# Optimization experiments

Measured on AMD Instinct MI355X. Metric: run time of the kernel, lower is better.

Reference implementation:

```python
import jax, jax.numpy as jnp
import numpy as np

NUM_NODES = 50000
NUM_EDGES = 800000
IN_CH = 64
HID = 64
SEQ = 8
K = 3
LAMBDA_MAX = 2.0  # PyG ChebConv default lambda_max for 'sym' normalization


def setup_inputs() -> dict:
    key = jax.random.key(0)
    ks = jax.random.split(key, 16)
    X = jax.random.normal(ks[0], (1, SEQ, NUM_NODES, IN_CH), dtype=jnp.float32)
    edge_index = jax.random.randint(ks[1], (2, NUM_EDGES), 0, NUM_NODES)
    edge_weight = jax.random.uniform(ks[2], (NUM_EDGES,), dtype=jnp.float32)

    def wb(i, cin):
        W = jax.random.normal(ks[3 + i], (K, cin, HID), dtype=jnp.float32) * 0.05
        b = jnp.zeros((HID,), dtype=jnp.float32)
        return W, b

    W_xz, b_xz = wb(0, IN_CH); W_hz, b_hz = wb(1, HID)
    W_xr, b_xr = wb(2, IN_CH); W_hr, b_hr = wb(3, HID)
    W_xh, b_xh = wb(4, IN_CH); W_hh, b_hh = wb(5, HID)
    return dict(X=X, edge_index=edge_index, edge_weight=edge_weight,
                W_xz=W_xz, b_xz=b_xz, W_hz=W_hz, b_hz=b_hz,
                W_xr=W_xr, b_xr=b_xr, W_hr=W_hr, b_hr=b_hr,
                W_xh=W_xh, b_xh=b_xh, W_hh=W_hh, b_hh=b_hh)


def _cheb_norm(edge_index, edge_weight, n):
    # Scaled Laplacian L_hat = (2/lambda_max) * (I - D^-1/2 A D^-1/2) - I
    row, col = edge_index[0], edge_index[1]
    w = jnp.where(row == col, 0.0, edge_weight)  # remove self loops (PyG does)
    deg = jax.ops.segment_sum(w, row, num_segments=n)
    dinv = jnp.where(deg > 0, jax.lax.rsqrt(jnp.where(deg > 0, deg, 1.0)), 0.0)
    wn = -(2.0 / LAMBDA_MAX) * w * dinv[row] * dinv[col]  # off-diagonal entries
    diag = 2.0 / LAMBDA_MAX - 1.0  # diagonal entry (0 for sym, lambda_max=2)
    return row, col, wn, diag


def _cheb_conv(x, W, b, row, col, wn, diag):
    # Chebyshev recurrence: T0 = x, T1 = L_hat x, T_k = 2 L_hat T_{k-1} - T_{k-2}
    n = x.shape[0]

    def prop(v):  # sparse L_hat @ v
        return jax.ops.segment_sum(wn[:, None] * v[col], row, num_segments=n) + diag * v

    out = x @ W[0]
    Tx_prev, Tx = x, prop(x)
    out = out + Tx @ W[1]
    for k in range(2, W.shape[0]):
        Tx_prev, Tx = Tx, 2.0 * prop(Tx) - Tx_prev
        out = out + Tx @ W[k]
    return out + b


def _gconv_gru(X, edge_index, edge_weight, params):
    B, L, N, C = X.shape
    row, col, wn, diag = _cheb_norm(edge_index, edge_weight, B * N)
    (W_xz, b_xz, W_hz, b_hz, W_xr, b_xr, W_hr, b_hr, W_xh, b_xh, W_hh, b_hh) = params
    hid = W_xz.shape[2]
    H0 = jnp.zeros((B * N, hid), dtype=X.dtype)

    def cc(v, W, b):
        return _cheb_conv(v, W, b, row, col, wn, diag)

    def step(H, Xt):  # Xt: [B, N, C] flattened per original reshape
        Xf = Xt.reshape(B * N, C)
        Z = jax.nn.sigmoid(cc(Xf, W_xz, b_xz) + cc(H, W_hz, b_hz))
        R = jax.nn.sigmoid(cc(Xf, W_xr, b_xr) + cc(H, W_hr, b_hr))
        Ht = jnp.tanh(cc(Xf, W_xh, b_xh) + cc(H * R, W_hh, b_hh))
        Hn = Z * H + (1.0 - Z) * Ht
        return Hn, Hn

    Hlast, states = jax.lax.scan(step, H0, jnp.moveaxis(X, 1, 0))
    States = jnp.moveaxis(states.reshape(L, B, N, hid), 0, 1)  # [B, L, N, hid]
    return States, Hlast.reshape(B, N, hid)


def reference(X, edge_index, edge_weight, W_xz, b_xz, W_hz, b_hz, W_xr, b_xr,
              W_hr, b_hr, W_xh, b_xh, W_hh, b_hh):
    params = (W_xz, b_xz, W_hz, b_hz, W_xr, b_xr, W_hr, b_hr, W_xh, b_xh, W_hh, b_hh)
    return _gconv_gru(X, edge_index, edge_weight, params)
```

## Files before the change

kernel.cpp:

```cpp
#include <hip/hip_runtime.h>
#include <cmath>

#define SEQLEN 8
#define CH 64

typedef unsigned short ushort_t;
typedef __attribute__((ext_vector_type(8))) short bf16x8;
typedef __attribute__((ext_vector_type(4))) float f32x4;

__device__ __forceinline__ ushort_t f2bf(float f) {
  union { float f; unsigned u; } v; v.f = f;
  unsigned r = v.u + 0x7fff + ((v.u >> 16) & 1);
  return (ushort_t)(r >> 16);
}
__device__ __forceinline__ float bf2f(ushort_t h) {
  union { unsigned u; float f; } v; v.u = ((unsigned)h) << 16;
  return v.f;
}

__global__ __launch_bounds__(256) void edge_hist_kernel(
    const int* __restrict__ ei, const float* __restrict__ ew,
    float* __restrict__ deg, int* __restrict__ cnt, int E) {
  int e = blockIdx.x * 256 + threadIdx.x;
  if (e >= E) return;
  int r = ei[e];
  int c = ei[E + e];
  float wv = (r == c) ? 0.f : ew[e];
  atomicAdd(deg + r, wv);
  atomicAdd(cnt + r, 1);
}

__global__ __launch_bounds__(256) void dinv_kernel(
    const float* __restrict__ deg, float* __restrict__ dinv, int n) {
  int i = blockIdx.x * 256 + threadIdx.x;
  if (i >= n) return;
  float d = deg[i];
  dinv[i] = (d > 0.f) ? (1.0f / sqrtf(d)) : 0.f;
}

__global__ __launch_bounds__(256) void scan_part_kernel(
    const int* __restrict__ cnt, int* __restrict__ bsum, int n) {
  int i = blockIdx.x * 256 + threadIdx.x;
  int v = (i < n) ? cnt[i] : 0;
#pragma unroll
  for (int o = 32; o; o >>= 1) v += __shfl_down(v, o, 64);
  __shared__ int red[4];
  if ((threadIdx.x & 63) == 0) red[threadIdx.x >> 6] = v;
  __syncthreads();
  if (threadIdx.x == 0) bsum[blockIdx.x] = red[0] + red[1] + red[2] + red[3];
}

__global__ __launch_bounds__(256) void scan_top_kernel(int* __restrict__ bsum, int nb) {
  int tid = threadIdx.x, lane = tid & 63, wid = tid >> 6;
  int v = (tid < nb) ? bsum[tid] : 0;
  int orig = v;
#pragma unroll
  for (int o = 1; o < 64; o <<= 1) { int t = __shfl_up(v, o, 64); if (lane >= o) v += t; }
  __shared__ int wsum[4];
  if (lane == 63) wsum[wid] = v;
  __syncthreads();
  int base = 0;
  for (int w = 0; w < wid; ++w) base += wsum[w];
  if (tid < nb) bsum[tid] = base + v - orig;
}

__global__ __launch_bounds__(256) void scan_fill_kernel(
    const int* __restrict__ cnt, const int* __restrict__ bsum,
    int* __restrict__ rowp, int* __restrict__ woff, int n, int total) {
  int i = blockIdx.x * 256 + threadIdx.x;
  int tid = threadIdx.x, lane = tid & 63, wid = tid >> 6;
  int v = (i < n) ? cnt[i] : 0;
  int orig = v;
#pragma unroll
  for (int o = 1; o < 64; o <<= 1) { int t = __shfl_up(v, o, 64); if (lane >= o) v += t; }
  __shared__ int wsum[4];
  if (lane == 63) wsum[wid] = v;
  __syncthreads();
  int base = bsum[blockIdx.x];
  for (int w = 0; w < wid; ++w) base += wsum[w];
  if (i < n) { int ex = base + v - orig; rowp[i] = ex; woff[i] = ex; }
  if (blockIdx.x == 0 && tid == 0) rowp[n] = total;
}

__global__ __launch_bounds__(256) void scatter_kernel(
    const int* __restrict__ ei, const float* __restrict__ ew,
    const float* __restrict__ dinv, int* __restrict__ woff,
    int* __restrict__ ccol, float* __restrict__ cwn, int E) {
  int e = blockIdx.x * 256 + threadIdx.x;
  if (e >= E) return;
  int r = ei[e];
  int c = ei[E + e];
  float wv = (r == c) ? 0.f : ew[e];
  float wn = -wv * dinv[r] * dinv[c];
  int pos = atomicAdd(woff + r, 1);
  ccol[pos] = c;
  cwn[pos] = wn;
}

__global__ __launch_bounds__(256) void cvt_bt_kernel(
    const float* __restrict__ X, ushort_t* __restrict__ Xt,
    long long NF, long long total4) {
  long long i = (long long)blockIdx.x * 256 + threadIdx.x;
  if (i >= total4) return;
  long long e4 = i * 4;
  int node = (int)(e4 >> 9);
  int rem = (int)(e4 & 511);
  int slab = rem >> 6;
  int cb = rem & 63;
  const float* src = X + (size_t)slab * NF + (size_t)node * CH + cb;
  float4 v = *(const float4*)src;
  ushort4 o;
  o.x = f2bf(v.x); o.y = f2bf(v.y); o.z = f2bf(v.z); o.w = f2bf(v.w);
  *(ushort4*)(Xt + e4) = o;
}

__global__ __launch_bounds__(256) void cvt_wt_kernel(
    const float* __restrict__ W, ushort_t* __restrict__ Wt) {
  int i = blockIdx.x * 256 + threadIdx.x;
  if (i >= 3 * 4096) return;
  int kk = i >> 12, rem = i & 4095, c = rem >> 6, k = rem & 63;
  Wt[i] = f2bf(W[(kk << 12) + (k << 6) + c]);
}

__global__ __launch_bounds__(256) void spmv_kernel(
    const int* __restrict__ rowp, const int* __restrict__ ccol,
    const float* __restrict__ cwn, const float* __restrict__ v,
    const float* __restrict__ u, float* __restrict__ y,
    float alpha, float beta, int n, long long slab_stride) {
  int r = blockIdx.x * 4 + (threadIdx.x >> 6);
  if (r >= n) return;
  long long so = (long long)blockIdx.y * slab_stride;
  const float* __restrict__ vs = v + so;
  const float* __restrict__ us = u + so;
  float* __restrict__ ys = y + so;
  int lane = threadIdx.x & 63;
  int s = __builtin_amdgcn_readfirstlane(rowp[r]);
  int e = __builtin_amdgcn_readfirstlane(rowp[r + 1]);
  float a0 = 0.f, a1 = 0.f, a2 = 0.f, a3 = 0.f;
  int i = s;
  for (; i + 4 <= e; i += 4) {
    int c0 = ccol[i], c1 = ccol[i + 1], c2 = ccol[i + 2], c3 = ccol[i + 3];
    float w0 = cwn[i], w1 = cwn[i + 1], w2 = cwn[i + 2], w3 = cwn[i + 3];
    float x0 = vs[(size_t)c0 * CH + lane];
    float x1 = vs[(size_t)c1 * CH + lane];
    float x2 = vs[(size_t)c2 * CH + lane];
    float x3 = vs[(size_t)c3 * CH + lane];
    a0 = fmaf(w0, x0, a0); a1 = fmaf(w1, x1, a1);
    a2 = fmaf(w2, x2, a2); a3 = fmaf(w3, x3, a3);
  }
  for (; i < e; ++i) a0 = fmaf(cwn[i], vs[(size_t)ccol[i] * CH + lane], a0);
  float res = alpha * ((a0 + a1) + (a2 + a3));
  if (beta != 0.f) res += beta * us[(size_t)r * CH + lane];
  ys[(size_t)r * CH + lane] = res;
}

__global__ __launch_bounds__(256) void spmv_bt_kernel(
    const int* __restrict__ rowp, const int* __restrict__ ccol,
    const float* __restrict__ cwn, const ushort_t* __restrict__ v,
    const float* __restrict__ u, ushort_t* __restrict__ yt,
    float alpha, float beta, int n, long long NF) {
  int r = blockIdx.x * 4 + (threadIdx.x >> 6);
  if (r >= n) return;
  int lane = threadIdx.x & 63;
  int s = __builtin_amdgcn_readfirstlane(rowp[r]);
  int e = __builtin_amdgcn_readfirstlane(rowp[r + 1]);
  float acc[8];
#pragma unroll
  for (int k = 0; k < 8; ++k) acc[k] = 0.f;
  const ushort_t* __restrict__ vl = v + (size_t)lane * 8;
  for (int i = s; i < e; i += 16) {
    int idxl = i + (lane & 15);
    int last = e - 1;
    if (idxl > last) idxl = last;
    int cL = ccol[idxl];
    float wL = cwn[idxl];
    int jv = e - i;
#pragma unroll
    for (int j = 0; j < 16; ++j) {
      int cj = __builtin_amdgcn_readlane(cL, j);
      int wb = __builtin_amdgcn_readlane(__float_as_int(wL), j);
      float wj = (j < jv) ? __int_as_float(wb) : 0.f;
      union { float4 f4; ushort_t us[8]; } tt;
      tt.f4 = *(const float4*)(vl + (size_t)cj * (SEQLEN * CH));
#pragma unroll
      for (int k = 0; k < 8; ++k)
        acc[k] = fmaf(wj, bf2f(tt.us[k]), acc[k]);
    }
  }
  float res[8];
#pragma unroll
  for (int k = 0; k < 8; ++k) res[k] = alpha * acc[k];
  if (beta != 0.f) {
    const float* up = u + (size_t)(lane >> 3) * NF + (size_t)r * CH + (size_t)(lane & 7) * 8;
    float4 ua = *(const float4*)up;
    float4 ub = *(const float4*)(up + 4);
    res[0] += beta * ua.x; res[1] += beta * ua.y; res[2] += beta * ua.z; res[3] += beta * ua.w;
    res[4] += beta * ub.x; res[5] += beta * ub.y; res[6] += beta * ub.z; res[7] += beta * ub.w;
  }
  union { float4 f4; ushort_t us[8]; } o;
#pragma unroll
  for (int k = 0; k < 8; ++k) o.us[k] = f2bf(res[k]);
  *(float4*)(yt + (size_t)r * (SEQLEN * CH) + (size_t)lane * 8) = o.f4;
}

__global__ __launch_bounds__(256) void spmv_bfx_kernel(
    const int* __restrict__ rowp, const int* __restrict__ ccol,
    const float* __restrict__ cwn, const ushort_t* __restrict__ v,
    const float* __restrict__ u, float* __restrict__ y, ushort_t* __restrict__ yb,
    float alpha, float beta, int n) {
  int r = blockIdx.x * 4 + (threadIdx.x >> 6);
  if (r >= n) return;
  int lane = threadIdx.x & 63;
  int s = __builtin_amdgcn_readfirstlane(rowp[r]);
  int e = __builtin_amdgcn_readfirstlane(rowp[r + 1]);
  float a0 = 0.f, a1 = 0.f, a2 = 0.f, a3 = 0.f;
  for (int i = s; i < e; i += 16) {
    int idxl = i + (lane & 15);
    int last = e - 1;
    if (idxl > last) idxl = last;
    int cL = ccol[idxl];
    float wL = cwn[idxl];
    int jv = e - i;
#pragma unroll
    for (int j = 0; j < 16; ++j) {
      int cj = __builtin_amdgcn_readlane(cL, j);
      int wb = __builtin_amdgcn_readlane(__float_as_int(wL), j);
      float wj = (j < jv) ? __int_as_float(wb) : 0.f;
      float xv = bf2f(v[(size_t)cj * CH + lane]);
      if ((j & 3) == 0) a0 = fmaf(wj, xv, a0);
      else if ((j & 3) == 1) a1 = fmaf(wj, xv, a1);
      else if ((j & 3) == 2) a2 = fmaf(wj, xv, a2);
      else a3 = fmaf(wj, xv, a3);
    }
  }
  float res = alpha * ((a0 + a1) + (a2 + a3));
  if (beta != 0.f) res += beta * u[(size_t)r * CH + lane];
  size_t oi = (size_t)r * CH + lane;
  if (y) y[oi] = res;
  if (yb) yb[oi] = f2bf(res);
}

__device__ __forceinline__ float sigf(float x) { return 1.f / (1.f + expf(-x)); }

struct FGM {
  const ushort_t* AB[3];
  const ushort_t* WB[3];
  const float* Bv[3];
  const float* P[2];
  const float* Hb;
  const float* Zb;
  float* O[3];
  ushort_t* OB0;
  int n;
  long long abstride;
};

template <int MODE, int G>
__global__ __launch_bounds__(256) void gemm_mfma_kernel(FGM p) {
  const int tid = threadIdx.x;
  const int wave = tid >> 6, lane = tid & 63;
  const int lr = lane & 15, kg = lane >> 4;
  const int wrow = blockIdx.x * 128 + wave * 32;
  f32x4 acc[G][2][4];
#pragma unroll
  for (int g = 0; g < G; ++g)
#pragma unroll
    for (int m = 0; m < 2; ++m)
#pragma unroll
      for (int ct = 0; ct < 4; ++ct) acc[g][m][ct] = (f32x4)0.f;

#pragma unroll
  for (int kk = 0; kk < 3; ++kk) {
    const ushort_t* __restrict__ Ab = p.AB[kk];
    bf16x8 a[2][2];
#pragma unroll
    for (int m = 0; m < 2; ++m) {
      int nn = wrow + m * 16 + lr;
      if (nn >= p.n) nn = p.n - 1;
      const ushort_t* ap = Ab + (size_t)nn * p.abstride + kg * 8;
      a[m][0] = *(const bf16x8*)(ap);
      a[m][1] = *(const bf16x8*)(ap + 32);
    }
#pragma unroll
    for (int g = 0; g < G; ++g) {
      const ushort_t* __restrict__ Wg = p.WB[g] + kk * 4096 + lr * 64 + kg * 8;
#pragma unroll
      for (int ct = 0; ct < 4; ++ct) {
        bf16x8 b0 = *(const bf16x8*)(Wg + ct * 1024);
        bf16x8 b1 = *(const bf16x8*)(Wg + ct * 1024 + 32);
        acc[g][0][ct] = __builtin_amdgcn_mfma_f32_16x16x32_bf16(a[0][0], b0, acc[g][0][ct], 0, 0, 0);
        acc[g][0][ct] = __builtin_amdgcn_mfma_f32_16x16x32_bf16(a[0][1], b1, acc[g][0][ct], 0, 0, 0);
        acc[g][1][ct] = __builtin_amdgcn_mfma_f32_16x16x32_bf16(a[1][0], b0, acc[g][1][ct], 0, 0, 0);
        acc[g][1][ct] = __builtin_amdgcn_mfma_f32_16x16x32_bf16(a[1][1], b1, acc[g][1][ct], 0, 0, 0);
      }
    }
  }

  if (MODE == 0) {
#pragma unroll
    for (int g = 0; g < G; ++g) {
#pragma unroll
      for (int ct = 0; ct < 4; ++ct) {
        int col = ct * 16 + lr;
        float bv = p.Bv[g][col];
#pragma unroll
        for (int m = 0; m < 2; ++m) {
#pragma unroll
          for (int i = 0; i < 4; ++i) {
            int row = wrow + m * 16 + kg * 4 + i;
            if (row < p.n) p.O[g][(size_t)row * CH + col] = acc[g][m][ct][i] + bv;
          }
        }
      }
    }
  } else if (MODE == 1) {
#pragma unroll
    for (int ct = 0; ct < 4; ++ct) {
      int col = ct * 16 + lr;
      float bz = p.Bv[0][col];
      float br = p.Bv[1][col];
#pragma unroll
      for (int m = 0; m < 2; ++m) {
#pragma unroll
        for (int i = 0; i < 4; ++i) {
          int row = wrow + m * 16 + kg * 4 + i;
          if (row < p.n) {
            size_t idx = (size_t)row * CH + col;
            float z = sigf(p.P[0][idx] + bz + acc[0][m][ct][i]);
            float gg = p.Hb[idx] * sigf(p.P[1][idx] + br + acc[1][m][ct][i]);
            p.O[0][idx] = z;
            p.O[1][idx] = gg;
            if (p.OB0) p.OB0[idx] = f2bf(gg);
          }
        }
      }
    }
  } else {
#pragma unroll
    for (int ct = 0; ct < 4; ++ct) {
      int col = ct * 16 + lr;
      float bh = p.Bv[0][col];
#pragma unroll
      for (int m = 0; m < 2; ++m) {
#pragma unroll
        for (int i = 0; i < 4; ++i) {
          int row = wrow + m * 16 + kg * 4 + i;
          if (row < p.n) {
            size_t idx = (size_t)row * CH + col;
            float tv = tanhf(p.P[0][idx] + bh + acc[0][m][ct][i]);
            float z4 = p.Zb[idx];
            float o = z4 * p.Hb[idx] + (1.f - z4) * tv;
            p.O[0][idx] = o;
            if (p.OB0) p.OB0[idx] = f2bf(o);
          }
        }
      }
    }
  }
}

struct FG {
  const float* A[3];
  const float* W[3];
  const float* Bv[3];
  const float* P[3];
  const float* Hb;
  const float* Zb;
  float* O[3];
  int n;
};

__device__ __forceinline__ void fma_tile(float (&acc)[4][4], const float* At,
                                         const float* Wt, int r0, int c0) {
#pragma unroll 4
  for (int k = 0; k < 64; ++k) {
    float4 a = *(const float4*)(At + k * 68 + r0);
    float4 w = *(const float4*)(Wt + k * 64 + c0);
    float av[4] = { a.x, a.y, a.z, a.w };
    float wv[4] = { w.x, w.y, w.z, w.w };
#pragma unroll
    for (int i = 0; i < 4; ++i)
#pragma unroll
      for (int j = 0; j < 4; ++j)
        acc[i][j] = fmaf(av[i], wv[j], acc[i][j]);
  }
}

template <int MODE, int G>
__global__ __launch_bounds__(256) void gemmf_kernel(FG p) {
  __shared__ float At[64 * 68];
  __shared__ float Wt[64 * 64];
  const int tid = threadIdx.x;
  const int n0 = blockIdx.x * 64;
  const int r0 = (tid >> 4) << 2;
  const int c0 = (tid & 15) << 2;
  float acc[G][4][4];
#pragma unroll
  for (int g = 0; g < G; ++g)
#pragma unroll
    for (int i = 0; i < 4; ++i)
#pragma unroll
      for (int j = 0; j < 4; ++j) acc[g][i][j] = 0.f;

  for (int kk = 0; kk < 3; ++kk) {
    const float* __restrict__ A = p.A[kk];
    __syncthreads();
#pragma unroll
    for (int j = 0; j < 4; ++j) {
      int flat = tid + 256 * j;
      int r = flat >> 4;
      int k4 = (flat & 15) << 2;
      int nn = n0 + r;
      float4 av = (nn < p.n) ? *(const float4*)(A + (size_t)nn * CH + k4)
                             : make_float4(0.f, 0.f, 0.f, 0.f);
      At[(k4 + 0) * 68 + r] = av.x;
      At[(k4 + 1) * 68 + r] = av.y;
      At[(k4 + 2) * 68 + r] = av.z;
      At[(k4 + 3) * 68 + r] = av.w;
    }
#pragma unroll
    for (int g = 0; g < G; ++g) {
      if (g > 0) __syncthreads();
      const float* __restrict__ Wk = p.W[g] + kk * 4096;
#pragma unroll
      for (int j = 0; j < 4; ++j) {
        int flat = tid + 256 * j;
        *(float4*)(Wt + flat * 4) = *(const float4*)(Wk + flat * 4);
      }
      __syncthreads();
      fma_tile(acc[g], At, Wt, r0, c0);
    }
  }

  if (MODE == 0) {
#pragma unroll
    for (int g = 0; g < G; ++g) {
      float4 bv = *(const float4*)(p.Bv[g] + c0);
#pragma unroll
      for (int i = 0; i < 4; ++i) {
        int nn = n0 + r0 + i;
        if (nn < p.n) {
          float4 o;
          o.x = acc[g][i][0] + bv.x;
          o.y = acc[g][i][1] + bv.y;
          o.z = acc[g][i][2] + bv.z;
          o.w = acc[g][i][3] + bv.w;
          *(float4*)(p.O[g] + (size_t)nn * CH + c0) = o;
        }
      }
    }
  } else if (MODE == 1) {
    float4 bz = *(const float4*)(p.Bv[0] + c0);
    float4 br = *(const float4*)(p.Bv[1] + c0);
#pragma unroll
    for (int i = 0; i < 4; ++i) {
      int nn = n0 + r0 + i;
      if (nn < p.n) {
        size_t idx = (size_t)nn * CH + c0;
        float4 pz = *(const float4*)(p.P[0] + idx);
        float4 pr = *(const float4*)(p.P[1] + idx);
        float4 h4 = *(const float4*)(p.Hb + idx);
        float4 z, gg;
        z.x = sigf(pz.x + bz.x + acc[0][i][0]);
        z.y = sigf(pz.y + bz.y + acc[0][i][1]);
        z.z = sigf(pz.z + bz.z + acc[0][i][2]);
        z.w = sigf(pz.w + bz.w + acc[0][i][3]);
        gg.x = h4.x * sigf(pr.x + br.x + acc[1][i][0]);
        gg.y = h4.y * sigf(pr.y + br.y + acc[1][i][1]);
        gg.z = h4.z * sigf(pr.z + br.z + acc[1][i][2]);
        gg.w = h4.w * sigf(pr.w + br.w + acc[1][i][3]);
        *(float4*)(p.O[0] + idx) = z;
        *(float4*)(p.O[1] + idx) = gg;
      }
    }
  } else {
    float4 bh = *(const float4*)(p.Bv[0] + c0);
#pragma unroll
    for (int i = 0; i < 4; ++i) {
      int nn = n0 + r0 + i;
      if (nn < p.n) {
        size_t idx = (size_t)nn * CH + c0;
        float4 ph = *(const float4*)(p.P[0] + idx);
        float4 z4 = *(const float4*)(p.Zb + idx);
        float4 h4 = *(const float4*)(p.Hb + idx);
        float4 o;
        float t0 = tanhf(ph.x + bh.x + acc[0][i][0]);
        float t1 = tanhf(ph.y + bh.y + acc[0][i][1]);
        float t2 = tanhf(ph.z + bh.z + acc[0][i][2]);
        float t3 = tanhf(ph.w + bh.w + acc[0][i][3]);
        o.x = z4.x * h4.x + (1.f - z4.x) * t0;
        o.y = z4.y * h4.y + (1.f - z4.y) * t1;
        o.z = z4.z * h4.z + (1.f - z4.z) * t2;
        o.w = z4.w * h4.w + (1.f - z4.w) * t3;
        *(float4*)(p.O[0] + idx) = o;
      }
    }
  }
}

__global__ __launch_bounds__(256) void t0_kernel(
    const float4* __restrict__ xzp, const float4* __restrict__ xhp,
    const float* __restrict__ b_hz, const float* __restrict__ b_hh,
    float4* __restrict__ out0, ushort_t* __restrict__ out0b, int n4) {
  int i = blockIdx.x * 256 + threadIdx.x;
  if (i >= n4) return;
  int cb = (i << 2) & 63;
  float4 bz = *(const float4*)(b_hz + cb);
  float4 bh = *(const float4*)(b_hh + cb);
  float4 z4 = xzp[i], h4 = xhp[i];
  float4 o;
  o.x = (1.f - sigf(z4.x + bz.x)) * tanhf(h4.x + bh.x);
  o.y = (1.f - sigf(z4.y + bz.y)) * tanhf(h4.y + bh.y);
  o.z = (1.f - sigf(z4.z + bz.z)) * tanhf(h4.z + bh.z);
  o.w = (1.f - sigf(z4.w + bz.w)) * tanhf(h4.w + bh.w);
  out0[i] = o;
  if (out0b) {
    ushort4 ob;
    ob.x = f2bf(o.x); ob.y = f2bf(o.y); ob.z = f2bf(o.z); ob.w = f2bf(o.w);
    *(ushort4*)(out0b + (size_t)i * 4) = ob;
  }
}

extern "C" void kernel_launch(void* const* d_in, const int* in_sizes, int n_in,
                              void* d_out, int out_size, void* d_ws, size_t ws_size,
                              hipStream_t stream) {
  const float* X    = (const float*)d_in[0];
  const int*   ei   = (const int*)d_in[1];
  const float* ewt  = (const float*)d_in[2];
  const float* W_xz = (const float*)d_in[3];  const float* b_xz = (const float*)d_in[4];
  const float* W_hz = (const float*)d_in[5];  const float* b_hz = (const float*)d_in[6];
  const float* W_xr = (const float*)d_in[7];  const float* b_xr = (const float*)d_in[8];
  const float* W_hr = (const float*)d_in[9];  const float* b_hr = (const float*)d_in[10];
  const float* W_xh = (const float*)d_in[11]; const float* b_xh = (const float*)d_in[12];
  const float* W_hh = (const float*)d_in[13]; const float* b_hh = (const float*)d_in[14];

  const int N = in_sizes[0] / (SEQLEN * CH);
  const int E = in_sizes[1] / 2;
  const size_t NF = (size_t)N * CH;
  float* out = (float*)d_out;

  char* base = (char*)d_ws;
  size_t off = 0;
  auto take = [&](size_t bytes) -> void* {
    off = (off + 255) & ~(size_t)255;
    void* p = base + off;
    off += bytes;
    return p;
  };
  float* deg   = (float*)take((size_t)N * 4);
  float* dinv  = (float*)take((size_t)N * 4);
  int*   cnt   = (int*)take((size_t)N * 4);
  int*   rowp  = (int*)take((size_t)(N + 1) * 4);
  int*   woff  = (int*)take((size_t)(N + 1) * 4);
  int*   bsum  = (int*)take(1024 * 4);
  int*   ccol  = (int*)take((size_t)E * 4);
  float* cwn   = (float*)take((size_t)E * 4);
  float* t1    = (float*)take(NF * 4);
  float* t2    = (float*)take(NF * 4);
  float* xz    = (float*)take(NF * 4);
  float* xr    = (float*)take(NF * 4);
  float* xh    = (float*)take(NF * 4);
  float* Gb    = (float*)take(NF * 4);
  ushort_t* Xb   = (ushort_t*)take(NF * 2 * SEQLEN);
  ushort_t* t1xb = (ushort_t*)take(NF * 2 * SEQLEN);
  ushort_t* t2xb = (ushort_t*)take(NF * 2 * SEQLEN);
  ushort_t* Hbb  = (ushort_t*)take(NF * 2);
  ushort_t* Gbb  = (ushort_t*)take(NF * 2);
  ushort_t* t1b  = (ushort_t*)take(NF * 2);
  ushort_t* t2b  = (ushort_t*)take(NF * 2);
  ushort_t* Wxzb = (ushort_t*)take(3 * 4096 * 2);
  ushort_t* Wxrb = (ushort_t*)take(3 * 4096 * 2);
  ushort_t* Wxhb = (ushort_t*)take(3 * 4096 * 2);
  ushort_t* Whzb = (ushort_t*)take(3 * 4096 * 2);
  ushort_t* Whrb = (ushort_t*)take(3 * 4096 * 2);
  ushort_t* Whhb = (ushort_t*)take(3 * 4096 * 2);
  size_t off_bf = off;
  (void)n_in; (void)out_size;
  const bool useBF = (off_bf <= ws_size);

  hipMemsetAsync(deg, 0, (size_t)N * 4, stream);
  hipMemsetAsync(cnt, 0, (size_t)N * 4, stream);

  const int ebl = (E + 255) / 256;
  const int nbl = (N + 255) / 256;
  edge_hist_kernel<<<ebl, 256, 0, stream>>>(ei, ewt, deg, cnt, E);
  dinv_kernel<<<nbl, 256, 0, stream>>>(deg, dinv, N);
  scan_part_kernel<<<nbl, 256, 0, stream>>>(cnt, bsum, N);
  scan_top_kernel<<<1, 256, 0, stream>>>(bsum, nbl);
  scan_fill_kernel<<<nbl, 256, 0, stream>>>(cnt, bsum, rowp, woff, N, E);
  scatter_kernel<<<ebl, 256, 0, stream>>>(ei, ewt, dinv, woff, ccol, cwn, E);

  const int nq = (N + 3) / 4;
  const int g3x = (N + 63) / 64;
  const int gmx = (N + 127) / 128;
  const int n4 = (int)(NF / 4);
  const int ewbl = (n4 + 255) / 256;

  if (useBF) {
    cvt_wt_kernel<<<48, 256, 0, stream>>>(W_xz, Wxzb);
    cvt_wt_kernel<<<48, 256, 0, stream>>>(W_xr, Wxrb);
    cvt_wt_kernel<<<48, 256, 0, stream>>>(W_xh, Wxhb);
    cvt_wt_kernel<<<48, 256, 0, stream>>>(W_hz, Whzb);
    cvt_wt_kernel<<<48, 256, 0, stream>>>(W_hr, Whrb);
    cvt_wt_kernel<<<48, 256, 0, stream>>>(W_hh, Whhb);

    long long xn4 = (long long)(NF * SEQLEN / 4);
    cvt_bt_kernel<<<(int)((xn4 + 255) / 256), 256, 0, stream>>>(X, Xb, (long long)NF, xn4);
    spmv_bt_kernel<<<dim3(nq, 1), 256, 0, stream>>>(
        rowp, ccol, cwn, Xb, nullptr, t1xb, 1.f, 0.f, N, (long long)NF);
    spmv_bt_kernel<<<dim3(nq, 1), 256, 0, stream>>>(
        rowp, ccol, cwn, t1xb, X, t2xb, 2.f, -1.f, N, (long long)NF);

    for (int t = 0; t < SEQLEN; ++t) {
      float* outt = out + (size_t)t * NF;

      FGM px = {};
      px.AB[0] = Xb + (size_t)t * CH;
      px.AB[1] = t1xb + (size_t)t * CH;
      px.AB[2] = t2xb + (size_t)t * CH;
      px.WB[0] = Wxzb; px.WB[1] = Wxrb; px.WB[2] = Wxhb;
      px.Bv[0] = b_xz; px.Bv[1] = b_xr; px.Bv[2] = b_xh;
      px.O[0] = xz; px.O[1] = xr; px.O[2] = xh;
      px.n = N; px.abstride = SEQLEN * CH;
      gemm_mfma_kernel<0, 3><<<dim3(gmx, 1, 1), 256, 0, stream>>>(px);

      if (t == 0) {
        t0_kernel<<<ewbl, 256, 0, stream>>>((const float4*)xz, (const float4*)xh,
                                            b_hz, b_hh, (float4*)outt, Hbb, n4);
        continue;
      }
      const float* H = out + (size_t)(t - 1) * NF;

      spmv_bfx_kernel<<<dim3(nq, 1), 256, 0, stream>>>(rowp, ccol, cwn, Hbb, H, t1, t1b, 1.f, 0.f, N);
      spmv_bfx_kernel<<<dim3(nq, 1), 256, 0, stream>>>(rowp, ccol, cwn, t1b, H, t2, t2b, 2.f, -1.f, N);
      FGM ph = {};
      ph.AB[0] = Hbb; ph.AB[1] = t1b; ph.AB[2] = t2b;
      ph.WB[0] = Whzb; ph.WB[1] = Whrb;
      ph.Bv[0] = b_hz; ph.Bv[1] = b_hr;
      ph.P[0] = xz; ph.P[1] = xr;
      ph.Hb = H;
      ph.O[0] = xz;
      ph.O[1] = Gb;
      ph.OB0 = Gbb;
      ph.n = N; ph.abstride = CH;
      gemm_mfma_kernel<1, 2><<<dim3(gmx, 1, 1), 256, 0, stream>>>(ph);

      spmv_bfx_kernel<<<dim3(nq, 1), 256, 0, stream>>>(rowp, ccol, cwn, Gbb, Gb, t1, t1b, 1.f, 0.f, N);
      spmv_bfx_kernel<<<dim3(nq, 1), 256, 0, stream>>>(rowp, ccol, cwn, t1b, Gb, t2, t2b, 2.f, -1.f, N);
      FGM pg = {};
      pg.AB[0] = Gbb; pg.AB[1] = t1b; pg.AB[2] = t2b;
      pg.WB[0] = Whhb;
      pg.Bv[0] = b_hh;
      pg.P[0] = xh;
      pg.Zb = xz;
      pg.Hb = H;
      pg.O[0] = outt;
      pg.OB0 = (t < SEQLEN - 1) ? Hbb : nullptr;
      pg.n = N; pg.abstride = CH;
      gemm_mfma_kernel<2, 1><<<dim3(gmx, 1, 1), 256, 0, stream>>>(pg);
    }
  } else {
    for (int t = 0; t < SEQLEN; ++t) {
      const float* Xt = X + (size_t)t * NF;
      float* outt = out + (size_t)t * NF;

      spmv_kernel<<<dim3(nq, 1), 256, 0, stream>>>(rowp, ccol, cwn, Xt, Xt, t1, 1.f, 0.f, N, 0);
      spmv_kernel<<<dim3(nq, 1), 256, 0, stream>>>(rowp, ccol, cwn, t1, Xt, t2, 2.f, -1.f, N, 0);
      FG px = {};
      px.A[0] = Xt; px.A[1] = t1; px.A[2] = t2;
      px.W[0] = W_xz; px.W[1] = W_xr; px.W[2] = W_xh;
      px.Bv[0] = b_xz; px.Bv[1] = b_xr; px.Bv[2] = b_xh;
      px.O[0] = xz; px.O[1] = xr; px.O[2] = xh;
      px.n = N;
      gemmf_kernel<0, 3><<<dim3(g3x, 1, 1), 256, 0, stream>>>(px);

      if (t == 0) {
        t0_kernel<<<ewbl, 256, 0, stream>>>((const float4*)xz, (const float4*)xh,
                                            b_hz, b_hh, (float4*)outt, nullptr, n4);
        continue;
      }
      const float* H = out + (size_t)(t - 1) * NF;

      spmv_kernel<<<dim3(nq, 1), 256, 0, stream>>>(rowp, ccol, cwn, H, H, t1, 1.f, 0.f, N, 0);
      spmv_kernel<<<dim3(nq, 1), 256, 0, stream>>>(rowp, ccol, cwn, t1, H, t2, 2.f, -1.f, N, 0);
      FG ph = {};
      ph.A[0] = H; ph.A[1] = t1; ph.A[2] = t2;
      ph.W[0] = W_hz; ph.W[1] = W_hr;
      ph.Bv[0] = b_hz; ph.Bv[1] = b_hr;
      ph.P[0] = xz; ph.P[1] = xr;
      ph.Hb = H;
      ph.O[0] = xz;
      ph.O[1] = Gb;
      ph.n = N;
      gemmf_kernel<1, 2><<<dim3(g3x, 1, 1), 256, 0, stream>>>(ph);

      spmv_kernel<<<dim3(nq, 1), 256, 0, stream>>>(rowp, ccol, cwn, Gb, Gb, t1, 1.f, 0.f, N, 0);
      spmv_kernel<<<dim3(nq, 1), 256, 0, stream>>>(rowp, ccol, cwn, t1, Gb, t2, 2.f, -1.f, N, 0);
      FG pg = {};
      pg.A[0] = Gb; pg.A[1] = t1; pg.A[2] = t2;
      pg.W[0] = W_hh;
      pg.Bv[0] = b_hh;
      pg.P[0] = xh;
      pg.Zb = xz;
      pg.Hb = H;
      pg.O[0] = outt;
      pg.n = N;
      gemmf_kernel<2, 1><<<dim3(g3x, 1, 1), 256, 0, stream>>>(pg);
    }
  }

  hipMemcpyAsync(out + (size_t)SEQLEN * NF, out + (size_t)(SEQLEN - 1) * NF,
                 NF * 4, hipMemcpyDeviceToDevice, stream);
}
```

Baseline: 2.071 ms.

## Fuse input-side Chebyshev GEMMs into the hidden-state gate GEMM kernels

Removes the separate per-step input GEMM that wrote xz/xr/xh to fp32 buffers. The X-side Chebyshev products are now accumulated directly in the same MFMA accumulators as the H-side products inside the gate kernels, and t=0 gets its own fused kernel that replaces t0_kernel. The SpMV calls also stop writing the unused fp32 t1/t2 outputs. This trades extra X-operand loads and MFMAs in each gate kernel for fewer launches and less fp32 intermediate traffic.

```diff
diff --git a/kernel.cpp b/kernel.cpp
--- a/kernel.cpp
+++ b/kernel.cpp
@@ -242,21 +242,24 @@
 
 __device__ __forceinline__ float sigf(float x) { return 1.f / (1.f + expf(-x)); }
 
-struct FGM {
-  const ushort_t* AB[3];
-  const ushort_t* WB[3];
-  const float* Bv[3];
-  const float* P[2];
+struct FGF {
+  const ushort_t* ABx[3];
+  const ushort_t* ABh[3];
+  const ushort_t* WX[2];
+  const ushort_t* WH[2];
+  const float* BX[2];
+  const float* BH[2];
   const float* Hb;
   const float* Zb;
-  float* O[3];
-  ushort_t* OB0;
+  float* O0;
+  float* O1;
+  ushort_t* OB;
   int n;
-  long long abstride;
 };
 
-template <int MODE, int G>
-__global__ __launch_bounds__(256) void gemm_mfma_kernel(FGM p) {
+template <int MODE>
+__global__ __launch_bounds__(256) void gemm_fused_kernel(FGF p) {
+  constexpr int G = (MODE == 2) ? 1 : 2;
   const int tid = threadIdx.x;
   const int wave = tid >> 6, lane = tid & 63;
   const int lr = lane & 15, kg = lane >> 4;
@@ -269,21 +272,19 @@
 #pragma unroll
       for (int ct = 0; ct < 4; ++ct) acc[g][m][ct] = (f32x4)0.f;
 
+  int nn0 = wrow + lr;       if (nn0 >= p.n) nn0 = p.n - 1;
+  int nn1 = wrow + 16 + lr;  if (nn1 >= p.n) nn1 = p.n - 1;
+
 #pragma unroll
   for (int kk = 0; kk < 3; ++kk) {
-    const ushort_t* __restrict__ Ab = p.AB[kk];
     bf16x8 a[2][2];
-#pragma unroll
-    for (int m = 0; m < 2; ++m) {
-      int nn = wrow + m * 16 + lr;
-      if (nn >= p.n) nn = p.n - 1;
-      const ushort_t* ap = Ab + (size_t)nn * p.abstride + kg * 8;
-      a[m][0] = *(const bf16x8*)(ap);
-      a[m][1] = *(const bf16x8*)(ap + 32);
-    }
+    const ushort_t* a0p = p.ABx[kk] + (size_t)nn0 * (SEQLEN * CH) + kg * 8;
+    const ushort_t* a1p = p.ABx[kk] + (size_t)nn1 * (SEQLEN * CH) + kg * 8;
+    a[0][0] = *(const bf16x8*)(a0p); a[0][1] = *(const bf16x8*)(a0p + 32);
+    a[1][0] = *(const bf16x8*)(a1p); a[1][1] = *(const bf16x8*)(a1p + 32);
 #pragma unroll
     for (int g = 0; g < G; ++g) {
-      const ushort_t* __restrict__ Wg = p.WB[g] + kk * 4096 + lr * 64 + kg * 8;
+      const ushort_t* __restrict__ Wg = p.WX[g] + kk * 4096 + lr * 64 + kg * 8;
 #pragma unroll
       for (int ct = 0; ct < 4; ++ct) {
         bf16x8 b0 = *(const bf16x8*)(Wg + ct * 1024);
@@ -296,65 +297,81 @@
     }
   }
 
-  if (MODE == 0) {
-#pragma unroll
-    for (int g = 0; g < G; ++g) {
-#pragma unroll
-      for (int ct = 0; ct < 4; ++ct) {
-        int col = ct * 16 + lr;
-        float bv = p.Bv[g][col];
-#pragma unroll
-        for (int m = 0; m < 2; ++m) {
-#pragma unroll
-          for (int i = 0; i < 4; ++i) {
-            int row = wrow + m * 16 + kg * 4 + i;
-            if (row < p.n) p.O[g][(size_t)row * CH + col] = acc[g][m][ct][i] + bv;
-          }
+  if (MODE != 0) {
+#pragma unroll
+    for (int kk = 0; kk < 3; ++kk) {
+      bf16x8 a[2][2];
+      const ushort_t* a0p = p.ABh[kk] + (size_t)nn0 * CH + kg * 8;
+      const ushort_t* a1p = p.ABh[kk] + (size_t)nn1 * CH + kg * 8;
+      a[0][0] = *(const bf16x8*)(a0p); a[0][1] = *(const bf16x8*)(a0p + 32);
+      a[1][0] = *(const bf16x8*)(a1p); a[1][1] = *(const bf16x8*)(a1p + 32);
+#pragma unroll
+      for (int g = 0; g < G; ++g) {
+        const ushort_t* __restrict__ Wg = p.WH[g] + kk * 4096 + lr * 64 + kg * 8;
+#pragma unroll
+        for (int ct = 0; ct < 4; ++ct) {
+          bf16x8 b0 = *(const bf16x8*)(Wg + ct * 1024);
+          bf16x8 b1 = *(const bf16x8*)(Wg + ct * 1024 + 32);
+          acc[g][0][ct] = __builtin_amdgcn_mfma_f32_16x16x32_bf16(a[0][0], b0, acc[g][0][ct], 0, 0, 0);
+          acc[g][0][ct] = __builtin_amdgcn_mfma_f32_16x16x32_bf16(a[0][1], b1, acc[g][0][ct], 0, 0, 0);
+          acc[g][1][ct] = __builtin_amdgcn_mfma_f32_16x16x32_bf16(a[1][0], b0, acc[g][1][ct], 0, 0, 0);
+          acc[g][1][ct] = __builtin_amdgcn_mfma_f32_16x16x32_bf16(a[1][1], b1, acc[g][1][ct], 0, 0, 0);
         }
       }
     }
-  } else if (MODE == 1) {
-#pragma unroll
-    for (int ct = 0; ct < 4; ++ct) {
-      int col = ct * 16 + lr;
-      float bz = p.Bv[0][col];
-      float br = p.Bv[1][col];
-#pragma unroll
-      for (int m = 0; m < 2; ++m) {
+  }
+
+#pragma unroll
+  for (int ct = 0; ct < 4; ++ct) {
+    int col = ct * 16 + lr;
+    if (MODE == 0) {
+      float bz = p.BX[0][col] + p.BH[0][col];
+      float bh = p.BX[1][col] + p.BH[1][col];
+#pragma unroll
+      for (int m = 0; m < 2; ++m)
 #pragma unroll
         for (int i = 0; i < 4; ++i) {
           int row = wrow + m * 16 + kg * 4 + i;
           if (row < p.n) {
             size_t idx = (size_t)row * CH + col;
-            float z = sigf(p.P[0][idx] + bz + acc[0][m][ct][i]);
-            float gg = p.Hb[idx] * sigf(p.P[1][idx] + br + acc[1][m][ct][i]);
-            p.O[0][idx] = z;
-            p.O[1][idx] = gg;
-            if (p.OB0) p.OB0[idx] = f2bf(gg);
+            float o = (1.f - sigf(acc[0][m][ct][i] + bz)) * tanhf(acc[1][m][ct][i] + bh);
+            p.O0[idx] = o;
+            p.OB[idx] = f2bf(o);
           }
         }
-      }
-    }
-  } else {
-#pragma unroll
-    for (int ct = 0; ct < 4; ++ct) {
-      int col = ct * 16 + lr;
-      float bh = p.Bv[0][col];
-#pragma unroll
-      for (int m = 0; m < 2; ++m) {
+    } else if (MODE == 1) {
+      float bz = p.BX[0][col] + p.BH[0][col];
+      float br = p.BX[1][col] + p.BH[1][col];
+#pragma unroll
+      for (int m = 0; m < 2; ++m)
 #pragma unroll
         for (int i = 0; i < 4; ++i) {
           int row = wrow + m * 16 + kg * 4 + i;
           if (row < p.n) {
             size_t idx = (size_t)row * CH + col;
-            float tv = tanhf(p.P[0][idx] + bh + acc[0][m][ct][i]);
-            float z4 = p.Zb[idx];
-            float o = z4 * p.Hb[idx] + (1.f - z4) * tv;
-            p.O[0][idx] = o;
-            if (p.OB0) p.OB0[idx] = f2bf(o);
+            float z = sigf(acc[0][m][ct][i] + bz);
+            float gg = p.Hb[idx] * sigf(acc[1][m][ct][i] + br);
+            p.O0[idx] = z;
+            p.O1[idx] = gg;
+            p.OB[idx] = f2bf(gg);
           }
         }
-      }
+    } else {
+      float bh = p.BX[0][col] + p.BH[0][col];
+#pragma unroll
+      for (int m = 0; m < 2; ++m)
+#pragma unroll
+        for (int i = 0; i < 4; ++i) {
+          int row = wrow + m * 16 + kg * 4 + i;
+          if (row < p.n) {
+            size_t idx = (size_t)row * CH + col;
+            float tv = tanhf(acc[0][m][ct][i] + bh);
+            float z = p.Zb[idx];
+            float o = z * p.Hb[idx] + (1.f - z) * tv;
+            p.O0[idx] = o;
+            if (p.OB) p.OB[idx] = f2bf(o);
+          }
+        }
     }
   }
 }
@@ -613,51 +630,56 @@
 
     for (int t = 0; t < SEQLEN; ++t) {
       float* outt = out + (size_t)t * NF;
-
-      FGM px = {};
-      px.AB[0] = Xb + (size_t)t * CH;
-      px.AB[1] = t1xb + (size_t)t * CH;
-      px.AB[2] = t2xb + (size_t)t * CH;
-      px.WB[0] = Wxzb; px.WB[1] = Wxrb; px.WB[2] = Wxhb;
-      px.Bv[0] = b_xz; px.Bv[1] = b_xr; px.Bv[2] = b_xh;
-      px.O[0] = xz; px.O[1] = xr; px.O[2] = xh;
-      px.n = N; px.abstride = SEQLEN * CH;
-      gemm_mfma_kernel<0, 3><<<dim3(gmx, 1, 1), 256, 0, stream>>>(px);
+      const ushort_t* Xs0 = Xb + (size_t)t * CH;
+      const ushort_t* Xs1 = t1xb + (size_t)t * CH;
+      const ushort_t* Xs2 = t2xb + (size_t)t * CH;
 
       if (t == 0) {
-        t0_kernel<<<ewbl, 256, 0, stream>>>((const float4*)xz, (const float4*)xh,
-                                            b_hz, b_hh, (float4*)outt, Hbb, n4);
+        FGF p0 = {};
+        p0.ABx[0] = Xs0; p0.ABx[1] = Xs1; p0.ABx[2] = Xs2;
+        p0.WX[0] = Wxzb; p0.WX[1] = Wxhb;
+        p0.BX[0] = b_xz; p0.BX[1] = b_xh;
+        p0.BH[0] = b_hz; p0.BH[1] = b_hh;
+        p0.O0 = outt; p0.OB = Hbb;
+        p0.n = N;
+        gemm_fused_kernel<0><<<dim3(gmx, 1, 1), 256, 0, stream>>>(p0);
         continue;
       }
       const float* H = out + (size_t)(t - 1) * NF;
 
-      spmv_bfx_kernel<<<dim3(nq, 1), 256, 0, stream>>>(rowp, ccol, cwn, Hbb, H, t1, t1b, 1.f, 0.f, N);
-      spmv_bfx_kernel<<<dim3(nq, 1), 256, 0, stream>>>(rowp, ccol, cwn, t1b, H, t2, t2b, 2.f, -1.f, N);
-      FGM ph = {};
-      ph.AB[0] = Hbb; ph.AB[1] = t1b; ph.AB[2] = t2b;
-      ph.WB[0] = Whzb; ph.WB[1] = Whrb;
-      ph.Bv[0] = b_hz; ph.Bv[1] = b_hr;
-      ph.P[0] = xz; ph.P[1] = xr;
-      ph.Hb = H;
-      ph.O[0] = xz;
-      ph.O[1] = Gb;
-      ph.OB0 = Gbb;
-      ph.n = N; ph.abstride = CH;
-      gemm_mfma_kernel<1, 2><<<dim3(gmx, 1, 1), 256, 0, stream>>>(ph);
-
-      spmv_bfx_kernel<<<dim3(nq, 1), 256, 0, stream>>>(rowp, ccol, cwn, Gbb, Gb, t1, t1b, 1.f, 0.f, N);
-      spmv_bfx_kernel<<<dim3(nq, 1), 256, 0, stream>>>(rowp, ccol, cwn, t1b, Gb, t2, t2b, 2.f, -1.f, N);
-      FGM pg = {};
-      pg.AB[0] = Gbb; pg.AB[1] = t1b; pg.AB[2] = t2b;
-      pg.WB[0] = Whhb;
-      pg.Bv[0] = b_hh;
-      pg.P[0] = xh;
-      pg.Zb = xz;
-      pg.Hb = H;
-      pg.O[0] = outt;
-      pg.OB0 = (t < SEQLEN - 1) ? Hbb : nullptr;
-      pg.n = N; pg.abstride = CH;
-      gemm_mfma_kernel<2, 1><<<dim3(gmx, 1, 1), 256, 0, stream>>>(pg);
+      spmv_bfx_kernel<<<dim3(nq, 1), 256, 0, stream>>>(rowp, ccol, cwn, Hbb, H, nullptr, t1b, 1.f, 0.f, N);
+      spmv_bfx_kernel<<<dim3(nq, 1), 256, 0, stream>>>(rowp, ccol, cwn, t1b, H, nullptr, t2b, 2.f, -1.f, N);
+
+      FGF p1 = {};
+      p1.ABx[0] = Xs0; p1.ABx[1] = Xs1; p1.ABx[2] = Xs2;
+      p1.ABh[0] = Hbb; p1.ABh[1] = t1b; p1.ABh[2] = t2b;
+      p1.WX[0] = Wxzb; p1.WX[1] = Wxrb;
+      p1.WH[0] = Whzb; p1.WH[1] = Whrb;
+      p1.BX[0] = b_xz; p1.BX[1] = b_xr;
+      p1.BH[0] = b_hz; p1.BH[1] = b_hr;
+      p1.Hb = H;
+      p1.O0 = xz;
+      p1.O1 = Gb;
+      p1.OB = Gbb;
+      p1.n = N;
+      gemm_fused_kernel<1><<<dim3(gmx, 1, 1), 256, 0, stream>>>(p1);
+
+      spmv_bfx_kernel<<<dim3(nq, 1), 256, 0, stream>>>(rowp, ccol, cwn, Gbb, Gb, nullptr, t1b, 1.f, 0.f, N);
+      spmv_bfx_kernel<<<dim3(nq, 1), 256, 0, stream>>>(rowp, ccol, cwn, t1b, Gb, nullptr, t2b, 2.f, -1.f, N);
+
+      FGF p2 = {};
+      p2.ABx[0] = Xs0; p2.ABx[1] = Xs1; p2.ABx[2] = Xs2;
+      p2.ABh[0] = Gbb; p2.ABh[1] = t1b; p2.ABh[2] = t2b;
+      p2.WX[0] = Wxhb;
+      p2.WH[0] = Whhb;
+      p2.BX[0] = b_xh;
+      p2.BH[0] = b_hh;
+      p2.Hb = H;
+      p2.Zb = xz;
+      p2.O0 = outt;
+      p2.OB = (t < SEQLEN - 1) ? Hbb : nullptr;
+      p2.n = N;
+      gemm_fused_kernel<2><<<dim3(gmx, 1, 1), 256, 0, stream>>>(p2);
     }
   } else {
     for (int t = 0; t < SEQLEN; ++t) {
```

Result: faster. 1.828 ms (-11.7%).
